# Optimization experiments

Measured on AMD Instinct MI355X. Metric: run time of the kernel, lower is better.

Reference implementation:

```python
import jax, jax.numpy as jnp
import numpy as np

# ViT-Base config
C, H, W = 3, 224, 224
NP = 14            # n_patches per side
PS = 16            # patch size (H // NP)
IN_D = C * PS * PS # 768
D = 768            # hidden_d
NH = 12            # n_heads
DH = D // NH       # 64
L = 12             # n_blocks
MLP = 4 * D        # mlp_ratio * hidden_d
OUT = 1000         # out_d
B = 64             # batch
S = NP * NP + 1    # 197 tokens (cls + patches)
EPS = 1e-5


def _pos_embed(seq_len, d):
    # get_positional_embeddings: sin on even dims, cos on odd dims
    i = jnp.arange(seq_len, dtype=jnp.float32)[:, None]
    j = jnp.arange(d, dtype=jnp.float32)[None, :]
    angle = i / jnp.power(10000.0, (j - j % 2) / d)
    return jnp.where(j % 2 == 0, jnp.sin(angle), jnp.cos(angle))


def _ln(x, g, b):
    m = x.mean(-1, keepdims=True)
    v = ((x - m) ** 2).mean(-1, keepdims=True)
    return (x - m) * jax.lax.rsqrt(v + EPS) * g + b


def _attn(x, qkv_w, qkv_b, out_w, out_b):
    n, s, _ = x.shape
    qkv = (x @ qkv_w + qkv_b).reshape(n, s, NH, 3, DH)  # matches torch chunk layout
    q, k, v = qkv[..., 0, :], qkv[..., 1, :], qkv[..., 2, :]
    scores = jnp.einsum('bqhd,bkhd->bhqk', q, k) / (DH ** 0.5)
    w = jax.nn.softmax(scores, axis=-1)
    o = jnp.einsum('bhqk,bkhd->bqhd', w, v).reshape(n, s, D)
    return o @ out_w + out_b


def setup_inputs() -> dict:
    key = jax.random.key(0)
    ks = jax.random.split(key, 16)
    sd = 0.02
    return {
        'images': jax.random.normal(ks[0], (B, C, H, W), jnp.float32),
        'lm_w': jax.random.normal(ks[1], (IN_D, D), jnp.float32) * sd,
        'lm_b': jnp.zeros((D,), jnp.float32),
        'cls_tok': jax.random.uniform(ks[2], (1, D), jnp.float32),
        'ln1_g': jnp.ones((L, D), jnp.float32),
        'ln1_b': jnp.zeros((L, D), jnp.float32),
        'qkv_w': jax.random.normal(ks[3], (L, D, 3 * D), jnp.float32) * sd,
        'qkv_b': jnp.zeros((L, 3 * D), jnp.float32),
        'out_w': jax.random.normal(ks[4], (L, D, D), jnp.float32) * sd,
        'out_b': jnp.zeros((L, D), jnp.float32),
        'ln2_g': jnp.ones((L, D), jnp.float32),
        'ln2_b': jnp.zeros((L, D), jnp.float32),
        'mlp1_w': jax.random.normal(ks[5], (L, D, MLP), jnp.float32) * sd,
        'mlp1_b': jnp.zeros((L, MLP), jnp.float32),
        'mlp2_w': jax.random.normal(ks[6], (L, MLP, D), jnp.float32) * sd,
        'mlp2_b': jnp.zeros((L, D), jnp.float32),
        'head_w': jax.random.normal(ks[7], (D, OUT), jnp.float32) * sd,
        'head_b': jnp.zeros((OUT,), jnp.float32),
    }


def reference(images, lm_w, lm_b, cls_tok, ln1_g, ln1_b, qkv_w, qkv_b,
              out_w, out_b, ln2_g, ln2_b, mlp1_w, mlp1_b, mlp2_w, mlp2_b,
              head_w, head_b):
    n = images.shape[0]
    # patchify: (N,C,H,W) -> (N, NP*NP, C*PS*PS), per-patch flatten order (C, ph, pw)
    p = images.reshape(n, C, NP, PS, NP, PS).transpose(0, 2, 4, 1, 3, 5)
    p = p.reshape(n, NP * NP, IN_D)
    tok = p @ lm_w + lm_b                                   # (N, 196, D)
    cls = jnp.broadcast_to(cls_tok, (n, 1, D))
    x = jnp.concatenate([cls, tok], axis=1) + _pos_embed(S, D)
    for l in range(L):
        x = x + _attn(_ln(x, ln1_g[l], ln1_b[l]), qkv_w[l], qkv_b[l], out_w[l], out_b[l])
        h = _ln(x, ln2_g[l], ln2_b[l])
        x = x + (jax.nn.gelu(h @ mlp1_w[l] + mlp1_b[l], approximate=False) @ mlp2_w[l] + mlp2_b[l])
    return jax.nn.softmax(x[:, 0] @ head_w + head_b, axis=-1)
```

## Files before the change

kernel.cpp:

```cpp
#include <hip/hip_runtime.h>
#include <hip/hip_bf16.h>
#include <math.h>

#define WS_B 64
#define WS_S 197
#define WS_D 768
#define WS_NH 12
#define WS_L 12
#define WS_MLP 3072
#define WS_OUT 1000
#define WS_IND 768
#define WS_NPAT 196
#define SP 208
#define JP 224

typedef __attribute__((ext_vector_type(8))) short bf16x8;
typedef __attribute__((ext_vector_type(4))) float f32x4;

static __device__ __forceinline__ float bf2f(short s) {
    unsigned u = ((unsigned)(unsigned short)s) << 16;
    return __builtin_bit_cast(float, u);
}
static __device__ __forceinline__ short f2bf(float f) {
    unsigned u = __builtin_bit_cast(unsigned, f);
    u = (u + 0x7FFF + ((u >> 16) & 1)) >> 16;
    return (short)u;
}

static __device__ __forceinline__ int xcd_remap(int wg, int nwg) {
    int q = nwg >> 3, r = nwg & 7;
    int xcd = wg & 7, idx = wg >> 3;
    return (xcd < r ? xcd * (q + 1) : r * (q + 1) + (xcd - r) * q) + idx;
}

__global__ __launch_bounds__(256) void wconv_kernel(
    const float* __restrict__ W, short* __restrict__ Wh, int K, int N)
{
    const int l = blockIdx.y;
    const float* Wl = W + (size_t)l * K * N;
    short* Whl = Wh + (size_t)l * N * K;
    int idx = blockIdx.x * 256 + threadIdx.x;
    int total = (K >> 3) * N;
    if (idx >= total) return;
    int n = idx % N, k8 = idx / N, k0 = k8 << 3;
    short hi[8];
#pragma unroll
    for (int j = 0; j < 8; ++j) hi[j] = f2bf(Wl[(size_t)(k0 + j) * N + n]);
    *(bf16x8*)(Whl + (size_t)n * K + k0) = *(bf16x8*)hi;
}

__global__ __launch_bounds__(256) void mfma_gemm(
    const short* __restrict__ A, int lda,
    const short* __restrict__ Bh,
    const float* __restrict__ bias, const float* __restrict__ res,
    float* __restrict__ outF, short* __restrict__ outH, int ldc,
    int M, int N, int K, int act)
{
    __shared__ short lds[32768];

    const int tid = threadIdx.x;
    const int w = tid >> 6, lane = tid & 63;
    const int nwg = gridDim.x * gridDim.y;
    int wg = blockIdx.y * gridDim.x + blockIdx.x;
    wg = xcd_remap(wg, nwg);
    const int bm = (wg / gridDim.x) * 128, bn = (wg % gridDim.x) * 128;
    const int wm = (w >> 1) * 64, wn = (w & 1) * 64;
    const int lr = lane & 15, lq = lane >> 4;

    f32x4 acc[4][4];
#pragma unroll
    for (int i = 0; i < 4; ++i)
#pragma unroll
        for (int j = 0; j < 4; ++j) acc[i][j] = (f32x4){0.f, 0.f, 0.f, 0.f};

    int aoff[2][4], boff[2][4];
#pragma unroll
    for (int ks = 0; ks < 2; ++ks)
#pragma unroll
        for (int f = 0; f < 4; ++f) {
            int r = wm + f * 16 + lr;
            aoff[ks][f] = r * 64 + (((ks * 4 + lq) ^ (lr & 7)) << 3);
            int rn = wn + f * 16 + lr;
            boff[ks][f] = rn * 64 + (((ks * 4 + lq) ^ (lr & 7)) << 3);
        }

    int srow[4], scs[4];
#pragma unroll
    for (int i = 0; i < 4; ++i) {
        int cid = i * 256 + tid;
        int row = cid >> 3, c = cid & 7;
        srow[i] = row;
        scs[i] = c ^ (row & 7);
    }

    const int nt = K >> 6;

    auto STAGE = [&](int kt, int slot) {
        const int k0 = kt << 6;
        short* Ab = &lds[slot * 8192];
        short* Bb = &lds[16384 + slot * 8192];
#pragma unroll
        for (int i = 0; i < 4; ++i) {
            int cid = i * 256 + tid;
            int arow = bm + srow[i]; if (arow >= M) arow = M - 1;
            const short* ga = A + (size_t)arow * lda + k0 + scs[i] * 8;
            __builtin_amdgcn_global_load_lds(
                (const __attribute__((address_space(1))) void*)ga,
                (__attribute__((address_space(3))) void*)(Ab + cid * 8), 16, 0, 0);
            const short* gb = Bh + (size_t)(bn + srow[i]) * K + k0 + scs[i] * 8;
            __builtin_amdgcn_global_load_lds(
                (const __attribute__((address_space(1))) void*)gb,
                (__attribute__((address_space(3))) void*)(Bb + cid * 8), 16, 0, 0);
        }
    };

    STAGE(0, 0);
    if (nt > 1) STAGE(1, 1);

    for (int t = 0; t < nt; ++t) {
        if (t + 1 < nt) asm volatile("s_waitcnt vmcnt(8)" ::: "memory");
        else            asm volatile("s_waitcnt vmcnt(0)" ::: "memory");
        asm volatile("s_barrier" ::: "memory");

        const short* Ab = &lds[(t & 1) * 8192];
        const short* Bb = &lds[16384 + (t & 1) * 8192];
#pragma unroll
        for (int ks = 0; ks < 2; ++ks) {
            bf16x8 av[4], bv[4];
#pragma unroll
            for (int f = 0; f < 4; ++f) av[f] = *(const bf16x8*)&Ab[aoff[ks][f]];
#pragma unroll
            for (int f = 0; f < 4; ++f) bv[f] = *(const bf16x8*)&Bb[boff[ks][f]];
            __builtin_amdgcn_s_setprio(1);
#pragma unroll
            for (int fm = 0; fm < 4; ++fm)
#pragma unroll
                for (int fn = 0; fn < 4; ++fn)
                    acc[fm][fn] = __builtin_amdgcn_mfma_f32_16x16x32_bf16(
                        av[fm], bv[fn], acc[fm][fn], 0, 0, 0);
            __builtin_amdgcn_s_setprio(0);
        }

        asm volatile("s_barrier" ::: "memory");
        if (t + 2 < nt) STAGE(t + 2, t & 1);
    }

#pragma unroll
    for (int fm = 0; fm < 4; ++fm)
#pragma unroll
        for (int fn = 0; fn < 4; ++fn) {
            int gc = bn + wn + fn * 16 + lr;
            float bvs = bias ? bias[gc] : 0.f;
            int grb = bm + wm + fm * 16 + lq * 4;
#pragma unroll
            for (int r = 0; r < 4; ++r) {
                int gr = grb + r;
                if (gr >= M) continue;
                float v = acc[fm][fn][r] + bvs;
                if (act == 1) v = 0.5f * v * (1.f + erff(v * 0.70710678118654752440f));
                if (res) v += res[(size_t)gr * ldc + gc];
                if (outF) outF[(size_t)gr * ldc + gc] = v;
                else      outH[(size_t)gr * ldc + gc] = f2bf(v);
            }
        }
}

__global__ __launch_bounds__(256) void attn_kernel(
    const short* __restrict__ qkv, short* __restrict__ o)
{
    __shared__ short Qs[SP * 64];
    __shared__ short Ks[SP * 64];
    __shared__ short Vt[64 * 256];
    __shared__ short Ps[4][16 * 256];

    const int bh = blockIdx.x;
    const int n = bh / WS_NH, h = bh % WS_NH;
    const short* base = qkv + (size_t)n * WS_S * 2304 + h * 192;
    const int tid = threadIdx.x;
    const int w = tid >> 6, lane = tid & 63;
    const int lr = lane & 15, lq = lane >> 4;

    const bf16x8 z8 = {0, 0, 0, 0, 0, 0, 0, 0};
    for (int i = lane; i < 512; i += 64) *(bf16x8*)&Ps[w][i * 8] = z8;

    for (int u = tid; u < SP * 8; u += 256) {
        int row = u >> 3, c = u & 7;
        int cs = c ^ (row & 7);
        bf16x8 vq = z8, vk = z8;
        if (row < WS_S) {
            const short* rp = base + (size_t)row * 2304;
            vq = *(const bf16x8*)(rp + cs * 8);
            vk = *(const bf16x8*)(rp + 64 + cs * 8);
        }
        *(bf16x8*)&Qs[row * 64 + c * 8] = vq;
        *(bf16x8*)&Ks[row * 64 + c * 8] = vk;
    }

#pragma unroll
    for (int pass = 0; pass < 7; ++pass) {
        int r = pass * 32 + (tid >> 3);
        int c = tid & 7;
        bf16x8 v = z8;
        if (r < WS_S) v = *(const bf16x8*)(base + (size_t)r * 2304 + 128 + c * 8);
#pragma unroll
        for (int e = 0; e < 8; ++e) {
            int d = c * 8 + e;
            Vt[d * 256 + ((((r >> 3)) ^ (d & 7)) << 3) + (r & 7)] = v[e];
        }
    }
    __syncthreads();

    for (int qt = w; qt < 13; qt += 4) {
        bf16x8 qv[2];
#pragma unroll
        for (int ks = 0; ks < 2; ++ks)
            qv[ks] = *(const bf16x8*)&Qs[(qt * 16 + lr) * 64 + (((ks * 4 + lq) ^ (lr & 7)) << 3)];
        f32x4 acc[13];
#pragma unroll
        for (int jt = 0; jt < 13; ++jt) acc[jt] = (f32x4){0.f, 0.f, 0.f, 0.f};
#pragma unroll
        for (int jt = 0; jt < 13; ++jt)
#pragma unroll
            for (int ks = 0; ks < 2; ++ks) {
                bf16x8 kv = *(const bf16x8*)&Ks[(jt * 16 + lr) * 64 + (((ks * 4 + lq) ^ (lr & 7)) << 3)];
                acc[jt] = __builtin_amdgcn_mfma_f32_16x16x32_bf16(kv, qv[ks], acc[jt], 0, 0, 0);
            }

        float s[13][4];
        float m = -1e30f;
#pragma unroll
        for (int jt = 0; jt < 13; ++jt)
#pragma unroll
            for (int r = 0; r < 4; ++r) {
                int j = jt * 16 + lq * 4 + r;
                float v = acc[jt][r] * 0.125f;
                s[jt][r] = v;
                if (j < WS_S) m = fmaxf(m, v);
            }
        m = fmaxf(m, __shfl_xor(m, 16));
        m = fmaxf(m, __shfl_xor(m, 32));
        float sum = 0.f;
#pragma unroll
        for (int jt = 0; jt < 13; ++jt)
#pragma unroll
            for (int r = 0; r < 4; ++r) {
                int j = jt * 16 + lq * 4 + r;
                float e = (j < WS_S) ? __expf(s[jt][r] - m) : 0.f;
                s[jt][r] = e;
                sum += e;
            }
        sum += __shfl_xor(sum, 16);
        sum += __shfl_xor(sum, 32);
        float inv = (sum > 0.f) ? 1.f / sum : 0.f;

#pragma unroll
        for (int jt = 0; jt < 13; ++jt) {
            int jb = jt * 16 + lq * 4;
            int cj = jb >> 3, e = jb & 7;
            int off = lr * 256 + ((cj ^ (lr & 7)) << 3) + e;
            unsigned p01 = (unsigned)(unsigned short)f2bf(s[jt][0] * inv) |
                           ((unsigned)(unsigned short)f2bf(s[jt][1] * inv) << 16);
            unsigned p23 = (unsigned)(unsigned short)f2bf(s[jt][2] * inv) |
                           ((unsigned)(unsigned short)f2bf(s[jt][3] * inv) << 16);
            *(unsigned*)&Ps[w][off] = p01;
            *(unsigned*)&Ps[w][off + 2] = p23;
        }
        __builtin_amdgcn_s_waitcnt(0);

        bf16x8 pa[7];
#pragma unroll
        for (int ks = 0; ks < 7; ++ks)
            pa[ks] = *(const bf16x8*)&Ps[w][lr * 256 + (((ks * 4 + lq) ^ (lr & 7)) << 3)];
#pragma unroll
        for (int dt = 0; dt < 4; ++dt) {
            f32x4 oacc = (f32x4){0.f, 0.f, 0.f, 0.f};
#pragma unroll
            for (int ks = 0; ks < 7; ++ks) {
                bf16x8 vb = *(const bf16x8*)&Vt[(dt * 16 + lr) * 256 + (((ks * 4 + lq) ^ (lr & 7)) << 3)];
                oacc = __builtin_amdgcn_mfma_f32_16x16x32_bf16(pa[ks], vb, oacc, 0, 0, 0);
            }
#pragma unroll
            for (int r = 0; r < 4; ++r) {
                int qg = qt * 16 + lq * 4 + r;
                if (qg < WS_S)
                    o[((size_t)n * WS_S + qg) * WS_D + h * 64 + dt * 16 + lr] = f2bf(oacc[r]);
            }
        }
    }
}

__global__ __launch_bounds__(256) void head_kernel(
    const float* __restrict__ x, const float* __restrict__ W,
    const float* __restrict__ bias, float* __restrict__ out)
{
    int c = blockIdx.x * 16 + (threadIdx.x & 15);
    int m = blockIdx.y * 16 + (threadIdx.x >> 4);
    if (c >= WS_OUT) return;
    const float* xr = x + (size_t)m * (WS_S * WS_D);
    float acc = bias[c];
    for (int k = 0; k < WS_D; ++k)
        acc = fmaf(xr[k], W[(size_t)k * WS_OUT + c], acc);
    out[(size_t)m * WS_OUT + c] = acc;
}

__global__ __launch_bounds__(256) void ln_kernel(
    const float* __restrict__ x, const float* __restrict__ g,
    const float* __restrict__ b, short* __restrict__ y)
{
    __shared__ float ssum[4], ssq[4];
    const int row = blockIdx.x;
    const int tid = threadIdx.x;
    const float* xr = x + (size_t)row * WS_D;
    float v0 = xr[tid], v1 = xr[tid + 256], v2 = xr[tid + 512];
    float s = v0 + v1 + v2;
    float q = v0 * v0 + v1 * v1 + v2 * v2;
#pragma unroll
    for (int off = 32; off > 0; off >>= 1) {
        s += __shfl_xor(s, off);
        q += __shfl_xor(q, off);
    }
    if ((tid & 63) == 0) { ssum[tid >> 6] = s; ssq[tid >> 6] = q; }
    __syncthreads();
    s = ssum[0] + ssum[1] + ssum[2] + ssum[3];
    q = ssq[0] + ssq[1] + ssq[2] + ssq[3];
    const float mean = s * (1.f / WS_D);
    const float var = q * (1.f / WS_D) - mean * mean;
    const float rstd = rsqrtf(var + 1e-5f);
    short* yr = y + (size_t)row * WS_D;
    yr[tid]       = f2bf((v0 - mean) * rstd * g[tid]       + b[tid]);
    yr[tid + 256] = f2bf((v1 - mean) * rstd * g[tid + 256] + b[tid + 256]);
    yr[tid + 512] = f2bf((v2 - mean) * rstd * g[tid + 512] + b[tid + 512]);
}

__global__ void pe_kernel(float* __restrict__ pe)
{
    int idx = blockIdx.x * 256 + threadIdx.x;
    if (idx >= WS_S * WS_D) return;
    int s = idx / WS_D, j = idx % WS_D;
    float expo = (float)(j & ~1) / (float)WS_D;
    float angle = (float)s * powf(10000.f, -expo);
    pe[idx] = (j & 1) ? cosf(angle) : sinf(angle);
}

__global__ void patchify_kernel(const float* __restrict__ img, short* __restrict__ p)
{
    int idx = blockIdx.x * 256 + threadIdx.x;
    const int total = WS_B * WS_NPAT * WS_IND;
    if (idx >= total) return;
    int pid = idx / WS_IND;
    int e = idx % WS_IND;
    int n = pid / WS_NPAT, patch = pid % WS_NPAT;
    int c = e >> 8, r = e & 255;
    int iy = r >> 4, ix = r & 15;
    int py = patch / 14, px = patch % 14;
    p[idx] = f2bf(img[(((size_t)n * 3 + c) * 224 + py * 16 + iy) * 224 + px * 16 + ix]);
}

__global__ void assemble_kernel(const float* __restrict__ tok, const float* __restrict__ cls,
                                const float* __restrict__ pe, float* __restrict__ x)
{
    int idx = blockIdx.x * 256 + threadIdx.x;
    const int total = WS_B * WS_S * WS_D;
    if (idx >= total) return;
    int row = idx / WS_D, d = idx % WS_D;
    int n = row / WS_S, s = row % WS_S;
    float v = (s == 0) ? cls[d] : tok[((size_t)n * WS_NPAT + (s - 1)) * WS_D + d];
    x[idx] = v + pe[s * WS_D + d];
}

__global__ __launch_bounds__(256) void softmax1000_kernel(
    const float* __restrict__ logits, float* __restrict__ out)
{
    __shared__ float rmax[4], rsum[4];
    const int row = blockIdx.x;
    const int tid = threadIdx.x;
    const float* lr = logits + (size_t)row * WS_OUT;
    float v[4];
    float mx = -INFINITY;
#pragma unroll
    for (int i = 0; i < 4; ++i) {
        int c = tid + i * 256;
        v[i] = (c < WS_OUT) ? lr[c] : -INFINITY;
        mx = fmaxf(mx, v[i]);
    }
#pragma unroll
    for (int off = 32; off > 0; off >>= 1) mx = fmaxf(mx, __shfl_xor(mx, off));
    if ((tid & 63) == 0) rmax[tid >> 6] = mx;
    __syncthreads();
    mx = fmaxf(fmaxf(rmax[0], rmax[1]), fmaxf(rmax[2], rmax[3]));
    float sum = 0.f;
#pragma unroll
    for (int i = 0; i < 4; ++i) {
        int c = tid + i * 256;
        v[i] = (c < WS_OUT) ? expf(v[i] - mx) : 0.f;
        sum += v[i];
    }
#pragma unroll
    for (int off = 32; off > 0; off >>= 1) sum += __shfl_xor(sum, off);
    if ((tid & 63) == 0) rsum[tid >> 6] = sum;
    __syncthreads();
    sum = rsum[0] + rsum[1] + rsum[2] + rsum[3];
    const float inv = 1.f / sum;
#pragma unroll
    for (int i = 0; i < 4; ++i) {
        int c = tid + i * 256;
        if (c < WS_OUT) out[(size_t)row * WS_OUT + c] = v[i] * inv;
    }
}

extern "C" void kernel_launch(void* const* d_in, const int* in_sizes, int n_in,
                              void* d_out, int out_size, void* d_ws, size_t ws_size,
                              hipStream_t stream)
{
    const float* images = (const float*)d_in[0];
    const float* lm_w   = (const float*)d_in[1];
    const float* lm_b   = (const float*)d_in[2];
    const float* cls    = (const float*)d_in[3];
    const float* ln1_g  = (const float*)d_in[4];
    const float* ln1_b  = (const float*)d_in[5];
    const float* qkv_w  = (const float*)d_in[6];
    const float* qkv_b  = (const float*)d_in[7];
    const float* out_w  = (const float*)d_in[8];
    const float* out_b  = (const float*)d_in[9];
    const float* ln2_g  = (const float*)d_in[10];
    const float* ln2_b  = (const float*)d_in[11];
    const float* mlp1_w = (const float*)d_in[12];
    const float* mlp1_b = (const float*)d_in[13];
    const float* mlp2_w = (const float*)d_in[14];
    const float* mlp2_b = (const float*)d_in[15];
    const float* head_w = (const float*)d_in[16];
    const float* head_b = (const float*)d_in[17];

    const int ROWS = WS_B * WS_S;
    char* wsb = (char*)d_ws;
    size_t off = 0;
    auto alloc = [&](size_t bytes) {
        void* p = wsb + off;
        off += (bytes + 255) & ~(size_t)255;
        return p;
    };
    float* pe     = (float*)alloc((size_t)WS_S * WS_D * 4);
    float* x      = (float*)alloc((size_t)ROWS * WS_D * 4);
    short* xh     = (short*)alloc((size_t)ROWS * WS_D * 2);
    short* qkvh   = (short*)alloc((size_t)ROWS * 2304 * 2);
    short* oh     = (short*)alloc((size_t)ROWS * WS_D * 2);
    short* hh     = (short*)alloc((size_t)ROWS * WS_MLP * 2);
    float* logits = (float*)alloc((size_t)WS_B * WS_OUT * 4);
    short* ph     = (short*)alloc((size_t)WS_B * WS_NPAT * WS_IND * 2);
    short* qW_all  = (short*)alloc((size_t)WS_L * WS_D * 2304 * 2);
    short* oW_all  = (short*)alloc((size_t)WS_L * WS_D * WS_D * 2);
    short* m1W_all = (short*)alloc((size_t)WS_L * WS_D * WS_MLP * 2);
    short* m2W_all = (short*)alloc((size_t)WS_L * WS_MLP * WS_D * 2);
    short* lmWh    = (short*)alloc((size_t)WS_IND * WS_D * 2);
    float* tok  = (float*)hh;

    pe_kernel<<<(WS_S * WS_D + 255) / 256, 256, 0, stream>>>(pe);
    patchify_kernel<<<(WS_B * WS_NPAT * WS_IND + 255) / 256, 256, 0, stream>>>(images, ph);
    wconv_kernel<<<dim3((WS_IND / 8 * WS_D + 255) / 256, 1), 256, 0, stream>>>(lm_w, lmWh, WS_IND, WS_D);
    wconv_kernel<<<dim3((WS_D / 8 * 2304 + 255) / 256, WS_L), 256, 0, stream>>>(qkv_w, qW_all, WS_D, 2304);
    wconv_kernel<<<dim3((WS_D / 8 * WS_D + 255) / 256, WS_L), 256, 0, stream>>>(out_w, oW_all, WS_D, WS_D);
    wconv_kernel<<<dim3((WS_D / 8 * WS_MLP + 255) / 256, WS_L), 256, 0, stream>>>(mlp1_w, m1W_all, WS_D, WS_MLP);
    wconv_kernel<<<dim3((WS_MLP / 8 * WS_D + 255) / 256, WS_L), 256, 0, stream>>>(mlp2_w, m2W_all, WS_MLP, WS_D);

    mfma_gemm<<<dim3(6, 98), 256, 0, stream>>>(
        ph, WS_IND, lmWh, lm_b, nullptr, tok, nullptr, WS_D,
        WS_B * WS_NPAT, WS_D, WS_IND, 0);
    assemble_kernel<<<(WS_B * WS_S * WS_D + 255) / 256, 256, 0, stream>>>(tok, cls, pe, x);

    for (int l = 0; l < WS_L; ++l) {
        ln_kernel<<<ROWS, 256, 0, stream>>>(x, ln1_g + l * WS_D, ln1_b + l * WS_D, xh);
        mfma_gemm<<<dim3(18, 99), 256, 0, stream>>>(
            xh, WS_D, qW_all + (size_t)l * WS_D * 2304, qkv_b + l * 2304,
            nullptr, nullptr, qkvh, 2304, ROWS, 2304, WS_D, 0);
        attn_kernel<<<WS_B * WS_NH, 256, 0, stream>>>(qkvh, oh);
        mfma_gemm<<<dim3(6, 99), 256, 0, stream>>>(
            oh, WS_D, oW_all + (size_t)l * WS_D * WS_D, out_b + l * WS_D,
            x, x, nullptr, WS_D, ROWS, WS_D, WS_D, 0);
        ln_kernel<<<ROWS, 256, 0, stream>>>(x, ln2_g + l * WS_D, ln2_b + l * WS_D, xh);
        mfma_gemm<<<dim3(24, 99), 256, 0, stream>>>(
            xh, WS_D, m1W_all + (size_t)l * WS_D * WS_MLP, mlp1_b + l * WS_MLP,
            nullptr, nullptr, hh, WS_MLP, ROWS, WS_MLP, WS_D, 1);
        mfma_gemm<<<dim3(6, 99), 256, 0, stream>>>(
            hh, WS_MLP, m2W_all + (size_t)l * WS_MLP * WS_D, mlp2_b + l * WS_D,
            x, x, nullptr, WS_D, ROWS, WS_D, WS_MLP, 0);
    }

    head_kernel<<<dim3((WS_OUT + 15) / 16, 4), 256, 0, stream>>>(x, head_w, head_b, logits);
    softmax1000_kernel<<<WS_B, 256, 0, stream>>>(logits, (float*)d_out);
}
```

Measured before the change: 6.456 ms.

## Use single-buffered GEMM staging and a one-wave-per-row vectorized LayerNorm

The GEMM drops its double-buffered LDS pipeline and s_setprio hints. It now loads one 64-wide K tile into single A/B buffers, waits for vmcnt(0), computes, and syncs twice per iteration. LayerNorm now gives each 64-lane wave one row, uses float4 loads and 4-wide bf16 stores, and removes the shared-memory cross-wave reduction. Lower LDS use may allow higher occupancy, but global loads no longer overlap MFMA compute, which risks slower GEMMs.

```diff
diff --git a/kernel.cpp b/kernel.cpp
--- a/kernel.cpp
+++ b/kernel.cpp
@@ -15,6 +15,7 @@
 #define JP 224
 
 typedef __attribute__((ext_vector_type(8))) short bf16x8;
+typedef __attribute__((ext_vector_type(4))) short s16x4;
 typedef __attribute__((ext_vector_type(4))) float f32x4;
 
 static __device__ __forceinline__ float bf2f(short s) {
@@ -56,7 +57,8 @@
     float* __restrict__ outF, short* __restrict__ outH, int ldc,
     int M, int N, int K, int act)
 {
-    __shared__ short lds[32768];
+    __shared__ short As[128 * 64];
+    __shared__ short Bs[128 * 64];
 
     const int tid = threadIdx.x;
     const int w = tid >> 6, lane = tid & 63;
@@ -84,65 +86,48 @@
             boff[ks][f] = rn * 64 + (((ks * 4 + lq) ^ (lr & 7)) << 3);
         }
 
-    int srow[4], scs[4];
+    const short* gaB[4];
+    const short* gbB[4];
+    int ldsb[4];
 #pragma unroll
     for (int i = 0; i < 4; ++i) {
-        int cid = i * 256 + tid;
-        int row = cid >> 3, c = cid & 7;
-        srow[i] = row;
-        scs[i] = c ^ (row & 7);
-    }
-
-    const int nt = K >> 6;
-
-    auto STAGE = [&](int kt, int slot) {
-        const int k0 = kt << 6;
-        short* Ab = &lds[slot * 8192];
-        short* Bb = &lds[16384 + slot * 8192];
+        int chunk = w * 64 + i * 256 + lane;
+        int row = chunk >> 3, c = chunk & 7;
+        int cs = c ^ (row & 7);
+        int arow = bm + row; if (arow >= M) arow = M - 1;
+        gaB[i] = A + (size_t)arow * lda + cs * 8;
+        gbB[i] = Bh + (size_t)(bn + row) * K + cs * 8;
+        ldsb[i] = chunk * 8;
+    }
+
+    for (int k0 = 0; k0 < K; k0 += 64) {
 #pragma unroll
         for (int i = 0; i < 4; ++i) {
-            int cid = i * 256 + tid;
-            int arow = bm + srow[i]; if (arow >= M) arow = M - 1;
-            const short* ga = A + (size_t)arow * lda + k0 + scs[i] * 8;
             __builtin_amdgcn_global_load_lds(
-                (const __attribute__((address_space(1))) void*)ga,
-                (__attribute__((address_space(3))) void*)(Ab + cid * 8), 16, 0, 0);
-            const short* gb = Bh + (size_t)(bn + srow[i]) * K + k0 + scs[i] * 8;
+                (const __attribute__((address_space(1))) void*)(gaB[i] + k0),
+                (__attribute__((address_space(3))) void*)(As + ldsb[i]), 16, 0, 0);
             __builtin_amdgcn_global_load_lds(
-                (const __attribute__((address_space(1))) void*)gb,
-                (__attribute__((address_space(3))) void*)(Bb + cid * 8), 16, 0, 0);
-        }
-    };
-
-    STAGE(0, 0);
-    if (nt > 1) STAGE(1, 1);
-
-    for (int t = 0; t < nt; ++t) {
-        if (t + 1 < nt) asm volatile("s_waitcnt vmcnt(8)" ::: "memory");
-        else            asm volatile("s_waitcnt vmcnt(0)" ::: "memory");
-        asm volatile("s_barrier" ::: "memory");
-
-        const short* Ab = &lds[(t & 1) * 8192];
-        const short* Bb = &lds[16384 + (t & 1) * 8192];
+                (const __attribute__((address_space(1))) void*)(gbB[i] + k0),
+                (__attribute__((address_space(3))) void*)(Bs + ldsb[i]), 16, 0, 0);
+        }
+        asm volatile("s_waitcnt vmcnt(0)" ::: "memory");
+        __syncthreads();
+
 #pragma unroll
         for (int ks = 0; ks < 2; ++ks) {
             bf16x8 av[4], bv[4];
 #pragma unroll
-            for (int f = 0; f < 4; ++f) av[f] = *(const bf16x8*)&Ab[aoff[ks][f]];
-#pragma unroll
-            for (int f = 0; f < 4; ++f) bv[f] = *(const bf16x8*)&Bb[boff[ks][f]];
-            __builtin_amdgcn_s_setprio(1);
+            for (int f = 0; f < 4; ++f) av[f] = *(const bf16x8*)&As[aoff[ks][f]];
+#pragma unroll
+            for (int f = 0; f < 4; ++f) bv[f] = *(const bf16x8*)&Bs[boff[ks][f]];
 #pragma unroll
             for (int fm = 0; fm < 4; ++fm)
 #pragma unroll
                 for (int fn = 0; fn < 4; ++fn)
                     acc[fm][fn] = __builtin_amdgcn_mfma_f32_16x16x32_bf16(
                         av[fm], bv[fn], acc[fm][fn], 0, 0, 0);
-            __builtin_amdgcn_s_setprio(0);
-        }
-
-        asm volatile("s_barrier" ::: "memory");
-        if (t + 2 < nt) STAGE(t + 2, t & 1);
+        }
+        __syncthreads();
     }
 
 #pragma unroll
@@ -307,29 +292,39 @@
     const float* __restrict__ x, const float* __restrict__ g,
     const float* __restrict__ b, short* __restrict__ y)
 {
-    __shared__ float ssum[4], ssq[4];
-    const int row = blockIdx.x;
-    const int tid = threadIdx.x;
+    const int row = blockIdx.x * 4 + (threadIdx.x >> 6);
+    const int lane = threadIdx.x & 63;
     const float* xr = x + (size_t)row * WS_D;
-    float v0 = xr[tid], v1 = xr[tid + 256], v2 = xr[tid + 512];
-    float s = v0 + v1 + v2;
-    float q = v0 * v0 + v1 * v1 + v2 * v2;
+    float4 v0 = *(const float4*)(xr + lane * 4);
+    float4 v1 = *(const float4*)(xr + 256 + lane * 4);
+    float4 v2 = *(const float4*)(xr + 512 + lane * 4);
+    float s = v0.x + v0.y + v0.z + v0.w + v1.x + v1.y + v1.z + v1.w
+            + v2.x + v2.y + v2.z + v2.w;
+    float q = v0.x * v0.x + v0.y * v0.y + v0.z * v0.z + v0.w * v0.w
+            + v1.x * v1.x + v1.y * v1.y + v1.z * v1.z + v1.w * v1.w
+            + v2.x * v2.x + v2.y * v2.y + v2.z * v2.z + v2.w * v2.w;
 #pragma unroll
     for (int off = 32; off > 0; off >>= 1) {
         s += __shfl_xor(s, off);
         q += __shfl_xor(q, off);
     }
-    if ((tid & 63) == 0) { ssum[tid >> 6] = s; ssq[tid >> 6] = q; }
-    __syncthreads();
-    s = ssum[0] + ssum[1] + ssum[2] + ssum[3];
-    q = ssq[0] + ssq[1] + ssq[2] + ssq[3];
     const float mean = s * (1.f / WS_D);
     const float var = q * (1.f / WS_D) - mean * mean;
     const float rstd = rsqrtf(var + 1e-5f);
     short* yr = y + (size_t)row * WS_D;
-    yr[tid]       = f2bf((v0 - mean) * rstd * g[tid]       + b[tid]);
-    yr[tid + 256] = f2bf((v1 - mean) * rstd * g[tid + 256] + b[tid + 256]);
-    yr[tid + 512] = f2bf((v2 - mean) * rstd * g[tid + 512] + b[tid + 512]);
+#pragma unroll
+    for (int c = 0; c < 3; ++c) {
+        int o = c * 256 + lane * 4;
+        float4 v = (c == 0) ? v0 : (c == 1) ? v1 : v2;
+        float4 gv = *(const float4*)(g + o);
+        float4 bv = *(const float4*)(b + o);
+        s16x4 ov;
+        ov[0] = f2bf((v.x - mean) * rstd * gv.x + bv.x);
+        ov[1] = f2bf((v.y - mean) * rstd * gv.y + bv.y);
+        ov[2] = f2bf((v.z - mean) * rstd * gv.z + bv.z);
+        ov[3] = f2bf((v.w - mean) * rstd * gv.w + bv.w);
+        *(s16x4*)(yr + o) = ov;
+    }
 }
 
 __global__ void pe_kernel(float* __restrict__ pe)
@@ -468,7 +463,7 @@
     assemble_kernel<<<(WS_B * WS_S * WS_D + 255) / 256, 256, 0, stream>>>(tok, cls, pe, x);
 
     for (int l = 0; l < WS_L; ++l) {
-        ln_kernel<<<ROWS, 256, 0, stream>>>(x, ln1_g + l * WS_D, ln1_b + l * WS_D, xh);
+        ln_kernel<<<ROWS / 4, 256, 0, stream>>>(x, ln1_g + l * WS_D, ln1_b + l * WS_D, xh);
         mfma_gemm<<<dim3(18, 99), 256, 0, stream>>>(
             xh, WS_D, qW_all + (size_t)l * WS_D * 2304, qkv_b + l * 2304,
             nullptr, nullptr, qkvh, 2304, ROWS, 2304, WS_D, 0);
@@ -476,7 +471,7 @@
         mfma_gemm<<<dim3(6, 99), 256, 0, stream>>>(
             oh, WS_D, oW_all + (size_t)l * WS_D * WS_D, out_b + l * WS_D,
             x, x, nullptr, WS_D, ROWS, WS_D, WS_D, 0);
-        ln_kernel<<<ROWS, 256, 0, stream>>>(x, ln2_g + l * WS_D, ln2_b + l * WS_D, xh);
+        ln_kernel<<<ROWS / 4, 256, 0, stream>>>(x, ln2_g + l * WS_D, ln2_b + l * WS_D, xh);
         mfma_gemm<<<dim3(24, 99), 256, 0, stream>>>(
             xh, WS_D, m1W_all + (size_t)l * WS_D * WS_MLP, mlp1_b + l * WS_MLP,
             nullptr, nullptr, hh, WS_MLP, ROWS, WS_MLP, WS_D, 1);
```

Result: faster. 5.851 ms (-9.4%).
